# Optimization experiments

Measured on AMD Instinct MI355X. Metric: run time of the kernel, lower is better.

The kernel has to match this reference:

```python
import jax, jax.numpy as jnp
import numpy as np

KERNEL_EPS = 1e-3   # generalized_kernel epsilon (performer)
Z_EPS = 1e-6        # LinearHopfieldCore eps


def _phi(x, proj):
    # generalized_kernel with relu: phi(x) = relu(d^{-0.25} * x @ P^T) + 1e-3
    # x: [B, L, H, D], proj: [M, D] -> [B, L, H, M]
    scale = x.shape[-1] ** -0.25
    return jax.nn.relu(jnp.einsum('blhd,md->blhm', x * scale, proj)) + KERNEL_EPS


def setup_inputs() -> dict:
    key = jax.random.key(0)
    kq, kk, kv, kp = jax.random.split(key, 4)
    B, L, H, D, M = 4, 4096, 16, 64, 256
    return {
        'q': jax.random.normal(kq, (B, L, H, D), dtype=jnp.float32),
        'k': jax.random.normal(kk, (B, L, H, D), dtype=jnp.float32),
        'v': jax.random.normal(kv, (B, L, H, D), dtype=jnp.float32),
        'projection_matrix': jax.random.normal(kp, (M, D), dtype=jnp.float32),
    }


def reference(q, k, v, projection_matrix):
    # Feature maps [B, L, H, M]
    Qf = _phi(q, projection_matrix)
    Kf = _phi(k, projection_matrix)
    # Linear attention (non-causal):
    # KV = sum_s K_s otimes V_s : [B, H, M, E]
    KV = jnp.einsum('bshm,bshe->bhme', Kf, v)
    # Z = 1 / (Q . (sum_s K_s + eps)) : [B, H, L]
    Ksum = jnp.sum(Kf, axis=1) + Z_EPS        # [B, H, M]
    Z = 1.0 / jnp.einsum('blhm,bhm->bhl', Qf, Ksum)
    # out = (Q @ KV) * Z : [B, L, H, E]
    out = jnp.einsum('bhme,blhm,bhl->blhe', KV, Qf, Z)
    return out
```

## Files before the change

### kernel.cpp

```cpp
#include <hip/hip_runtime.h>


#define LL 4096
#define HH 16
#define DD 64
#define EE 64
#define MM 256
#define SCALE 0.35355339059327378f

typedef __attribute__((ext_vector_type(8))) __bf16 bf8v;
typedef __attribute__((ext_vector_type(4))) __bf16 bf4v;
typedef __attribute__((ext_vector_type(4))) float f4v;

__device__ __forceinline__ __bf16 f2bf(float f) {
  union { float f; unsigned u; } x; x.f = f;
  unsigned r = (x.u + 0x7FFFu + ((x.u >> 16) & 1u)) >> 16;
  union { unsigned short s; __bf16 b; } y; y.s = (unsigned short)r;
  return y.b;
}

#define MFMA16(a, b, c) __builtin_amdgcn_mfma_f32_16x16x32_bf16(a, b, c, 0, 0, 0)

#define KV_ELEMS (64 * 64 * 256)
#define KSUM_OFF KV_ELEMS
#define WS_ZERO_BYTES ((size_t)(KV_ELEMS + 64 * 256) * 4)

__global__ __launch_bounds__(256, 2)
void k1_kv(const float* __restrict__ kin, const float* __restrict__ vin,
           const float* __restrict__ pin, float* __restrict__ ws) {
  __shared__ __bf16 kt[64 * 72];
  __shared__ __bf16 vt[64 * 68];
  __shared__ __bf16 kft[256 * 72];

  const int tid = threadIdx.x;
  const int wave = tid >> 6;
  const int lane = tid & 63;
  const int qd = lane >> 4;
  const int nn = lane & 15;
  const int bh = blockIdx.y;
  const int b = bh >> 4, h = bh & 15;
  const int l0 = blockIdx.x * 512;

  bf8v pf[4][2];
#pragma unroll
  for (int mt = 0; mt < 4; ++mt) {
    const float* pr = pin + (size_t)(64 * wave + mt * 16 + nn) * DD;
#pragma unroll
    for (int c = 0; c < 2; ++c) {
      bf8v t;
#pragma unroll
      for (int j = 0; j < 8; ++j) t[j] = f2bf(pr[c * 32 + qd * 8 + j] * SCALE);
      pf[mt][c] = t;
    }
  }

  f4v acc[4][4];
#pragma unroll
  for (int i = 0; i < 4; ++i)
#pragma unroll
    for (int j = 0; j < 4; ++j) acc[i][j] = (f4v){0.f, 0.f, 0.f, 0.f};
  float ksum[4] = {0.f, 0.f, 0.f, 0.f};

  const size_t bhbase = (size_t)b * LL * HH * DD + (size_t)h * DD;
  const int srow = tid >> 2;
  const int scol = (tid & 3) * 16;

  for (int it = 0; it < 8; ++it) {
    {
      const size_t g = bhbase + (size_t)(l0 + it * 64 + srow) * (HH * DD) + scol;
      const f4v* gk = (const f4v*)(kin + g);
      const f4v* gv = (const f4v*)(vin + g);
      f4v k0 = gk[0], k1 = gk[1], k2 = gk[2], k3 = gk[3];
      f4v v0 = gv[0], v1 = gv[1], v2 = gv[2], v3 = gv[3];
      bf8v w0, w1;
#pragma unroll
      for (int j = 0; j < 4; ++j) {
        w0[j] = f2bf(k0[j]); w0[j + 4] = f2bf(k1[j]);
        w1[j] = f2bf(k2[j]); w1[j + 4] = f2bf(k3[j]);
      }
      *(bf8v*)&kt[srow * 72 + scol] = w0;
      *(bf8v*)&kt[srow * 72 + scol + 8] = w1;
      bf4v x0, x1, x2, x3;
#pragma unroll
      for (int j = 0; j < 4; ++j) {
        x0[j] = f2bf(v0[j]); x1[j] = f2bf(v1[j]);
        x2[j] = f2bf(v2[j]); x3[j] = f2bf(v3[j]);
      }
      *(bf4v*)&vt[srow * 68 + scol] = x0;
      *(bf4v*)&vt[srow * 68 + scol + 4] = x1;
      *(bf4v*)&vt[srow * 68 + scol + 8] = x2;
      *(bf4v*)&vt[srow * 68 + scol + 12] = x3;
    }
    __syncthreads();

#pragma unroll
    for (int lt = 0; lt < 4; ++lt) {
      bf8v a0 = *(const bf8v*)&kt[(lt * 16 + nn) * 72 + qd * 8];
      bf8v a1 = *(const bf8v*)&kt[(lt * 16 + nn) * 72 + 32 + qd * 8];
#pragma unroll
      for (int mt = 0; mt < 4; ++mt) {
        f4v cc = (f4v){0.f, 0.f, 0.f, 0.f};
        cc = MFMA16(a0, pf[mt][0], cc);
        cc = MFMA16(a1, pf[mt][1], cc);
        bf4v pk;
#pragma unroll
        for (int r = 0; r < 4; ++r) {
          float ph = fmaxf(cc[r], 0.f) + 1e-3f;
          ksum[mt] += ph;
          pk[r] = f2bf(ph);
        }
        *(bf4v*)&kft[(64 * wave + mt * 16 + nn) * 72 + lt * 16 + qd * 4] = pk;
      }
    }

#pragma unroll
    for (int c = 0; c < 2; ++c) {
      bf8v af[4];
#pragma unroll
      for (int mt = 0; mt < 4; ++mt)
        af[mt] = *(const bf8v*)&kft[(64 * wave + mt * 16 + nn) * 72 + c * 32 + qd * 8];
#pragma unroll
      for (int et = 0; et < 4; ++et) {
        bf8v bv;
#pragma unroll
        for (int j = 0; j < 8; ++j) bv[j] = vt[(c * 32 + qd * 8 + j) * 68 + et * 16 + nn];
#pragma unroll
        for (int mt = 0; mt < 4; ++mt) acc[mt][et] = MFMA16(af[mt], bv, acc[mt][et]);
      }
    }
    __syncthreads();
  }

  float* kvb = ws + (size_t)bh * (64 * 256);
#pragma unroll
  for (int mt = 0; mt < 4; ++mt)
#pragma unroll
    for (int et = 0; et < 4; ++et) {
#pragma unroll
      for (int r = 0; r < 4; ++r) {
        int m = 64 * wave + mt * 16 + 4 * qd + r;
        int e = et * 16 + nn;
        atomicAdd(&kvb[e * 256 + m], acc[mt][et][r]);
      }
    }
#pragma unroll
  for (int mt = 0; mt < 4; ++mt) {
    float s = ksum[mt];
    s += __shfl_xor(s, 16, 64);
    s += __shfl_xor(s, 32, 64);
    if (lane < 16) atomicAdd(&ws[KSUM_OFF + bh * 256 + 64 * wave + mt * 16 + lane], s);
  }
}

__global__ __launch_bounds__(256, 2)
void k3_out(const float* __restrict__ qin, const float* __restrict__ pin,
            const float* __restrict__ ws, float* __restrict__ out) {
  __shared__ __bf16 qt[64 * 72];
  __shared__ __bf16 qf[64 * 264];
  __shared__ float denp[256];
  __shared__ float denr[64];
  __shared__ float ksume[256];

  const int tid = threadIdx.x;
  const int wave = tid >> 6;
  const int lane = tid & 63;
  const int qd = lane >> 4;
  const int nn = lane & 15;
  const int bh = blockIdx.y;
  const int b = bh >> 4, h = bh & 15;
  const int l0 = blockIdx.x * 512;

  bf8v pf[4][2];
#pragma unroll
  for (int mt = 0; mt < 4; ++mt) {
    const float* pr = pin + (size_t)(64 * wave + mt * 16 + nn) * DD;
#pragma unroll
    for (int c = 0; c < 2; ++c) {
      bf8v t;
#pragma unroll
      for (int j = 0; j < 8; ++j) t[j] = f2bf(pr[c * 32 + qd * 8 + j] * SCALE);
      pf[mt][c] = t;
    }
  }

  const float* kvb = ws + (size_t)bh * (64 * 256);
  bf8v kvf[8];
#pragma unroll
  for (int c = 0; c < 8; ++c) {
    const float* src = kvb + (size_t)(16 * wave + nn) * 256 + c * 32 + qd * 8;
    bf8v t;
#pragma unroll
    for (int j = 0; j < 8; ++j) t[j] = f2bf(src[j]);
    kvf[c] = t;
  }

  ksume[tid] = ws[KSUM_OFF + bh * 256 + tid] + 1e-6f;

  const size_t bhbase = (size_t)b * LL * HH * DD + (size_t)h * DD;
  const int srow = tid >> 2;
  const int scol = (tid & 3) * 16;

  for (int it = 0; it < 8; ++it) {
    {
      const f4v* gq = (const f4v*)(qin + bhbase + (size_t)(l0 + it * 64 + srow) * (HH * DD) + scol);
      f4v q0 = gq[0], q1 = gq[1], q2 = gq[2], q3 = gq[3];
      bf8v w0, w1;
#pragma unroll
      for (int j = 0; j < 4; ++j) {
        w0[j] = f2bf(q0[j]); w0[j + 4] = f2bf(q1[j]);
        w1[j] = f2bf(q2[j]); w1[j + 4] = f2bf(q3[j]);
      }
      *(bf8v*)&qt[srow * 72 + scol] = w0;
      *(bf8v*)&qt[srow * 72 + scol + 8] = w1;
    }
    __syncthreads();

#pragma unroll
    for (int lt = 0; lt < 4; ++lt) {
      bf8v b0 = *(const bf8v*)&qt[(lt * 16 + nn) * 72 + qd * 8];
      bf8v b1 = *(const bf8v*)&qt[(lt * 16 + nn) * 72 + 32 + qd * 8];
      float dpart = 0.f;
#pragma unroll
      for (int mt = 0; mt < 4; ++mt) {
        f4v cc = (f4v){0.f, 0.f, 0.f, 0.f};
        cc = MFMA16(pf[mt][0], b0, cc);
        cc = MFMA16(pf[mt][1], b1, cc);
        bf4v pk;
#pragma unroll
        for (int r = 0; r < 4; ++r) {
          float ph = fmaxf(cc[r], 0.f) + 1e-3f;
          dpart += ph * ksume[64 * wave + mt * 16 + 4 * qd + r];
          pk[r] = f2bf(ph);
        }
        *(bf4v*)&qf[(lt * 16 + nn) * 264 + 64 * wave + mt * 16 + 4 * qd] = pk;
      }
      dpart += __shfl_xor(dpart, 16, 64);
      dpart += __shfl_xor(dpart, 32, 64);
      if (lane < 16) denp[wave * 64 + lt * 16 + lane] = dpart;
    }
    __syncthreads();
    if (tid < 64)
      denr[tid] = 1.f / (denp[tid] + denp[64 + tid] + denp[128 + tid] + denp[192 + tid]);
    __syncthreads();

#pragma unroll
    for (int lt = 0; lt < 4; ++lt) {
      f4v co = (f4v){0.f, 0.f, 0.f, 0.f};
#pragma unroll
      for (int c = 0; c < 8; ++c) {
        bf8v af = *(const bf8v*)&qf[(lt * 16 + nn) * 264 + c * 32 + qd * 8];
        co = MFMA16(af, kvf[c], co);
      }
#pragma unroll
      for (int r = 0; r < 4; ++r) {
        int lrel = lt * 16 + 4 * qd + r;
        int labs = l0 + it * 64 + lrel;
        out[((size_t)((size_t)b * LL + labs) * HH + h) * EE + 16 * wave + nn] =
            co[r] * denr[lrel];
      }
    }
    __syncthreads();
  }
}

extern "C" void kernel_launch(void* const* d_in, const int* in_sizes, int n_in,
                              void* d_out, int out_size, void* d_ws, size_t ws_size,
                              hipStream_t stream) {
  (void)in_sizes; (void)n_in; (void)out_size;
  const float* q = (const float*)d_in[0];
  const float* k = (const float*)d_in[1];
  const float* v = (const float*)d_in[2];
  const float* p = (const float*)d_in[3];
  float* ws = (float*)d_ws;
  float* out = (float*)d_out;

  if (ws_size < WS_ZERO_BYTES) return;

  hipMemsetAsync(d_ws, 0, WS_ZERO_BYTES, stream);
  dim3 grid(8, 64), blk(256);
  k1_kv<<<grid, blk, 0, stream>>>(k, v, p, ws);
  k3_out<<<grid, blk, 0, stream>>>(q, p, ws, out);
}
```

Before: 332.9 us.

## Double waves per block, prefetch next tile into registers, trim k3 barriers

Both kernels move from 4 to 8 waves per 512-thread block. In k1 each wave now owns 32 feature rows instead of 64. In k3 the waves split the L tiles, and each also covers its quarter of the E outputs. The global loads for the next 64-row tile are issued right after the barrier, so they overlap the MFMA work of the current tile. k3 also drops the separate reciprocal-denominator stage and the end-of-loop barrier, and each lane sums the four partial denominators itself. The aim is more latency hiding and fewer barrier stalls, at the cost of higher per-CU register pressure under the new launch bounds.

```diff
diff --git a/kernel.cpp b/kernel.cpp
--- a/kernel.cpp
+++ b/kernel.cpp
@@ -10,6 +10,7 @@
 
 typedef __attribute__((ext_vector_type(8))) __bf16 bf8v;
 typedef __attribute__((ext_vector_type(4))) __bf16 bf4v;
+typedef __attribute__((ext_vector_type(2))) __bf16 bf2v;
 typedef __attribute__((ext_vector_type(4))) float f4v;
 
 __device__ __forceinline__ __bf16 f2bf(float f) {
@@ -25,15 +26,15 @@
 #define KSUM_OFF KV_ELEMS
 #define WS_ZERO_BYTES ((size_t)(KV_ELEMS + 64 * 256) * 4)
 
-__global__ __launch_bounds__(256, 2)
+__global__ __launch_bounds__(512, 4)
 void k1_kv(const float* __restrict__ kin, const float* __restrict__ vin,
            const float* __restrict__ pin, float* __restrict__ ws) {
   __shared__ __bf16 kt[64 * 72];
-  __shared__ __bf16 vt[64 * 68];
+  __shared__ __bf16 vt[64 * 66];
   __shared__ __bf16 kft[256 * 72];
 
   const int tid = threadIdx.x;
-  const int wave = tid >> 6;
+  const int w = tid >> 6;
   const int lane = tid & 63;
   const int qd = lane >> 4;
   const int nn = lane & 15;
@@ -41,10 +42,19 @@
   const int b = bh >> 4, h = bh & 15;
   const int l0 = blockIdx.x * 512;
 
-  bf8v pf[4][2];
-#pragma unroll
-  for (int mt = 0; mt < 4; ++mt) {
-    const float* pr = pin + (size_t)(64 * wave + mt * 16 + nn) * DD;
+  const size_t bhbase = (size_t)b * LL * HH * DD + (size_t)h * DD;
+  const int srow = tid >> 3;
+  const int scol = (tid & 7) * 8;
+
+  const float* gk = kin + bhbase + (size_t)(l0 + srow) * (HH * DD) + scol;
+  const float* gv = vin + bhbase + (size_t)(l0 + srow) * (HH * DD) + scol;
+  f4v pk0 = ((const f4v*)gk)[0], pk1 = ((const f4v*)gk)[1];
+  f4v pv0 = ((const f4v*)gv)[0], pv1 = ((const f4v*)gv)[1];
+
+  bf8v pf[2][2];
+#pragma unroll
+  for (int mt = 0; mt < 2; ++mt) {
+    const float* pr = pin + (size_t)(32 * w + mt * 16 + nn) * DD;
 #pragma unroll
     for (int c = 0; c < 2; ++c) {
       bf8v t;
@@ -54,51 +64,42 @@
     }
   }
 
-  f4v acc[4][4];
-#pragma unroll
-  for (int i = 0; i < 4; ++i)
+  f4v acc[2][4];
+#pragma unroll
+  for (int i = 0; i < 2; ++i)
 #pragma unroll
     for (int j = 0; j < 4; ++j) acc[i][j] = (f4v){0.f, 0.f, 0.f, 0.f};
-  float ksum[4] = {0.f, 0.f, 0.f, 0.f};
-
-  const size_t bhbase = (size_t)b * LL * HH * DD + (size_t)h * DD;
-  const int srow = tid >> 2;
-  const int scol = (tid & 3) * 16;
+  float ksum[2] = {0.f, 0.f};
 
   for (int it = 0; it < 8; ++it) {
     {
-      const size_t g = bhbase + (size_t)(l0 + it * 64 + srow) * (HH * DD) + scol;
-      const f4v* gk = (const f4v*)(kin + g);
-      const f4v* gv = (const f4v*)(vin + g);
-      f4v k0 = gk[0], k1 = gk[1], k2 = gk[2], k3 = gk[3];
-      f4v v0 = gv[0], v1 = gv[1], v2 = gv[2], v3 = gv[3];
-      bf8v w0, w1;
-#pragma unroll
-      for (int j = 0; j < 4; ++j) {
-        w0[j] = f2bf(k0[j]); w0[j + 4] = f2bf(k1[j]);
-        w1[j] = f2bf(k2[j]); w1[j + 4] = f2bf(k3[j]);
-      }
-      *(bf8v*)&kt[srow * 72 + scol] = w0;
-      *(bf8v*)&kt[srow * 72 + scol + 8] = w1;
-      bf4v x0, x1, x2, x3;
-#pragma unroll
-      for (int j = 0; j < 4; ++j) {
-        x0[j] = f2bf(v0[j]); x1[j] = f2bf(v1[j]);
-        x2[j] = f2bf(v2[j]); x3[j] = f2bf(v3[j]);
-      }
-      *(bf4v*)&vt[srow * 68 + scol] = x0;
-      *(bf4v*)&vt[srow * 68 + scol + 4] = x1;
-      *(bf4v*)&vt[srow * 68 + scol + 8] = x2;
-      *(bf4v*)&vt[srow * 68 + scol + 12] = x3;
-    }
-    __syncthreads();
+      bf8v wk;
+#pragma unroll
+      for (int j = 0; j < 4; ++j) { wk[j] = f2bf(pk0[j]); wk[j + 4] = f2bf(pk1[j]); }
+      *(bf8v*)&kt[srow * 72 + scol] = wk;
+      bf2v x0 = {f2bf(pv0[0]), f2bf(pv0[1])};
+      bf2v x1 = {f2bf(pv0[2]), f2bf(pv0[3])};
+      bf2v x2 = {f2bf(pv1[0]), f2bf(pv1[1])};
+      bf2v x3 = {f2bf(pv1[2]), f2bf(pv1[3])};
+      *(bf2v*)&vt[srow * 66 + scol]     = x0;
+      *(bf2v*)&vt[srow * 66 + scol + 2] = x1;
+      *(bf2v*)&vt[srow * 66 + scol + 4] = x2;
+      *(bf2v*)&vt[srow * 66 + scol + 6] = x3;
+    }
+    __syncthreads();
+
+    if (it < 7) {
+      gk += 64 * HH * DD; gv += 64 * HH * DD;
+      pk0 = ((const f4v*)gk)[0]; pk1 = ((const f4v*)gk)[1];
+      pv0 = ((const f4v*)gv)[0]; pv1 = ((const f4v*)gv)[1];
+    }
 
 #pragma unroll
     for (int lt = 0; lt < 4; ++lt) {
       bf8v a0 = *(const bf8v*)&kt[(lt * 16 + nn) * 72 + qd * 8];
       bf8v a1 = *(const bf8v*)&kt[(lt * 16 + nn) * 72 + 32 + qd * 8];
 #pragma unroll
-      for (int mt = 0; mt < 4; ++mt) {
+      for (int mt = 0; mt < 2; ++mt) {
         f4v cc = (f4v){0.f, 0.f, 0.f, 0.f};
         cc = MFMA16(a0, pf[mt][0], cc);
         cc = MFMA16(a1, pf[mt][1], cc);
@@ -109,23 +110,21 @@
           ksum[mt] += ph;
           pk[r] = f2bf(ph);
         }
-        *(bf4v*)&kft[(64 * wave + mt * 16 + nn) * 72 + lt * 16 + qd * 4] = pk;
+        *(bf4v*)&kft[(32 * w + mt * 16 + nn) * 72 + lt * 16 + qd * 4] = pk;
       }
     }
 
 #pragma unroll
     for (int c = 0; c < 2; ++c) {
-      bf8v af[4];
-#pragma unroll
-      for (int mt = 0; mt < 4; ++mt)
-        af[mt] = *(const bf8v*)&kft[(64 * wave + mt * 16 + nn) * 72 + c * 32 + qd * 8];
+      bf8v af0 = *(const bf8v*)&kft[(32 * w + nn) * 72 + c * 32 + qd * 8];
+      bf8v af1 = *(const bf8v*)&kft[(32 * w + 16 + nn) * 72 + c * 32 + qd * 8];
 #pragma unroll
       for (int et = 0; et < 4; ++et) {
         bf8v bv;
 #pragma unroll
-        for (int j = 0; j < 8; ++j) bv[j] = vt[(c * 32 + qd * 8 + j) * 68 + et * 16 + nn];
-#pragma unroll
-        for (int mt = 0; mt < 4; ++mt) acc[mt][et] = MFMA16(af[mt], bv, acc[mt][et]);
+        for (int j = 0; j < 8; ++j) bv[j] = vt[(c * 32 + qd * 8 + j) * 66 + et * 16 + nn];
+        acc[0][et] = MFMA16(af0, bv, acc[0][et]);
+        acc[1][et] = MFMA16(af1, bv, acc[1][et]);
       }
     }
     __syncthreads();
@@ -133,47 +132,56 @@
 
   float* kvb = ws + (size_t)bh * (64 * 256);
 #pragma unroll
-  for (int mt = 0; mt < 4; ++mt)
+  for (int mt = 0; mt < 2; ++mt)
 #pragma unroll
     for (int et = 0; et < 4; ++et) {
 #pragma unroll
       for (int r = 0; r < 4; ++r) {
-        int m = 64 * wave + mt * 16 + 4 * qd + r;
+        int m = 32 * w + mt * 16 + 4 * qd + r;
         int e = et * 16 + nn;
         atomicAdd(&kvb[e * 256 + m], acc[mt][et][r]);
       }
     }
 #pragma unroll
-  for (int mt = 0; mt < 4; ++mt) {
+  for (int mt = 0; mt < 2; ++mt) {
     float s = ksum[mt];
     s += __shfl_xor(s, 16, 64);
     s += __shfl_xor(s, 32, 64);
-    if (lane < 16) atomicAdd(&ws[KSUM_OFF + bh * 256 + 64 * wave + mt * 16 + lane], s);
-  }
-}
-
-__global__ __launch_bounds__(256, 2)
+    if (lane < 16) atomicAdd(&ws[KSUM_OFF + bh * 256 + 32 * w + mt * 16 + lane], s);
+  }
+}
+
+__global__ __launch_bounds__(512, 4)
 void k3_out(const float* __restrict__ qin, const float* __restrict__ pin,
             const float* __restrict__ ws, float* __restrict__ out) {
   __shared__ __bf16 qt[64 * 72];
   __shared__ __bf16 qf[64 * 264];
   __shared__ float denp[256];
-  __shared__ float denr[64];
   __shared__ float ksume[256];
 
   const int tid = threadIdx.x;
-  const int wave = tid >> 6;
+  const int w = tid >> 6;
+  const int wm = w & 3;
+  const int wl = w >> 2;
   const int lane = tid & 63;
   const int qd = lane >> 4;
   const int nn = lane & 15;
   const int bh = blockIdx.y;
   const int b = bh >> 4, h = bh & 15;
   const int l0 = blockIdx.x * 512;
+  const int lt0 = 2 * wl;
+
+  const size_t bhbase = (size_t)b * LL * HH * DD + (size_t)h * DD;
+  const int srow = tid >> 3;
+  const int scol = (tid & 7) * 8;
+
+  const float* gq = qin + bhbase + (size_t)(l0 + srow) * (HH * DD) + scol;
+  f4v pq0 = ((const f4v*)gq)[0], pq1 = ((const f4v*)gq)[1];
 
   bf8v pf[4][2];
 #pragma unroll
   for (int mt = 0; mt < 4; ++mt) {
-    const float* pr = pin + (size_t)(64 * wave + mt * 16 + nn) * DD;
+    const float* pr = pin + (size_t)(64 * wm + mt * 16 + nn) * DD;
 #pragma unroll
     for (int c = 0; c < 2; ++c) {
       bf8v t;
@@ -187,36 +195,32 @@
   bf8v kvf[8];
 #pragma unroll
   for (int c = 0; c < 8; ++c) {
-    const float* src = kvb + (size_t)(16 * wave + nn) * 256 + c * 32 + qd * 8;
+    const float* src = kvb + (size_t)(16 * wm + nn) * 256 + c * 32 + qd * 8;
     bf8v t;
 #pragma unroll
     for (int j = 0; j < 8; ++j) t[j] = f2bf(src[j]);
     kvf[c] = t;
   }
 
-  ksume[tid] = ws[KSUM_OFF + bh * 256 + tid] + 1e-6f;
-
-  const size_t bhbase = (size_t)b * LL * HH * DD + (size_t)h * DD;
-  const int srow = tid >> 2;
-  const int scol = (tid & 3) * 16;
+  if (tid < 256) ksume[tid] = ws[KSUM_OFF + bh * 256 + tid] + 1e-6f;
 
   for (int it = 0; it < 8; ++it) {
     {
-      const f4v* gq = (const f4v*)(qin + bhbase + (size_t)(l0 + it * 64 + srow) * (HH * DD) + scol);
-      f4v q0 = gq[0], q1 = gq[1], q2 = gq[2], q3 = gq[3];
-      bf8v w0, w1;
-#pragma unroll
-      for (int j = 0; j < 4; ++j) {
-        w0[j] = f2bf(q0[j]); w0[j + 4] = f2bf(q1[j]);
-        w1[j] = f2bf(q2[j]); w1[j + 4] = f2bf(q3[j]);
-      }
-      *(bf8v*)&qt[srow * 72 + scol] = w0;
-      *(bf8v*)&qt[srow * 72 + scol + 8] = w1;
-    }
-    __syncthreads();
-
-#pragma unroll
-    for (int lt = 0; lt < 4; ++lt) {
+      bf8v wq;
+#pragma unroll
+      for (int j = 0; j < 4; ++j) { wq[j] = f2bf(pq0[j]); wq[j + 4] = f2bf(pq1[j]); }
+      *(bf8v*)&qt[srow * 72 + scol] = wq;
+    }
+    __syncthreads();
+
+    if (it < 7) {
+      gq += 64 * HH * DD;
+      pq0 = ((const f4v*)gq)[0]; pq1 = ((const f4v*)gq)[1];
+    }
+
+#pragma unroll
+    for (int li = 0; li < 2; ++li) {
+      const int lt = lt0 + li;
       bf8v b0 = *(const bf8v*)&qt[(lt * 16 + nn) * 72 + qd * 8];
       bf8v b1 = *(const bf8v*)&qt[(lt * 16 + nn) * 72 + 32 + qd * 8];
       float dpart = 0.f;
@@ -229,37 +233,39 @@
 #pragma unroll
         for (int r = 0; r < 4; ++r) {
           float ph = fmaxf(cc[r], 0.f) + 1e-3f;
-          dpart += ph * ksume[64 * wave + mt * 16 + 4 * qd + r];
+          dpart += ph * ksume[64 * wm + mt * 16 + 4 * qd + r];
           pk[r] = f2bf(ph);
         }
-        *(bf4v*)&qf[(lt * 16 + nn) * 264 + 64 * wave + mt * 16 + 4 * qd] = pk;
+        *(bf4v*)&qf[(lt * 16 + nn) * 264 + 64 * wm + mt * 16 + 4 * qd] = pk;
       }
       dpart += __shfl_xor(dpart, 16, 64);
       dpart += __shfl_xor(dpart, 32, 64);
-      if (lane < 16) denp[wave * 64 + lt * 16 + lane] = dpart;
-    }
-    __syncthreads();
-    if (tid < 64)
-      denr[tid] = 1.f / (denp[tid] + denp[64 + tid] + denp[128 + tid] + denp[192 + tid]);
-    __syncthreads();
-
-#pragma unroll
-    for (int lt = 0; lt < 4; ++lt) {
+      if (lane < 16) denp[wm * 64 + lt * 16 + lane] = dpart;
+    }
+    __syncthreads();
+
+#pragma unroll
+    for (int li = 0; li < 2; ++li) {
+      const int lt = lt0 + li;
       f4v co = (f4v){0.f, 0.f, 0.f, 0.f};
 #pragma unroll
       for (int c = 0; c < 8; ++c) {
         bf8v af = *(const bf8v*)&qf[(lt * 16 + nn) * 264 + c * 32 + qd * 8];
         co = MFMA16(af, kvf[c], co);
       }
+      f4v d0 = *(const f4v*)&denp[0 * 64 + lt * 16 + 4 * qd];
+      f4v d1 = *(const f4v*)&denp[1 * 64 + lt * 16 + 4 * qd];
+      f4v d2 = *(const f4v*)&denp[2 * 64 + lt * 16 + 4 * qd];
+      f4v d3 = *(const f4v*)&denp[3 * 64 + lt * 16 + 4 * qd];
 #pragma unroll
       for (int r = 0; r < 4; ++r) {
         int lrel = lt * 16 + 4 * qd + r;
         int labs = l0 + it * 64 + lrel;
-        out[((size_t)((size_t)b * LL + labs) * HH + h) * EE + 16 * wave + nn] =
-            co[r] * denr[lrel];
-      }
-    }
-    __syncthreads();
+        float rden = 1.f / (d0[r] + d1[r] + d2[r] + d3[r]);
+        out[((size_t)((size_t)b * LL + labs) * HH + h) * EE + 16 * wm + nn] =
+            co[r] * rden;
+      }
+    }
   }
 }
 
@@ -277,7 +283,7 @@
   if (ws_size < WS_ZERO_BYTES) return;
 
   hipMemsetAsync(d_ws, 0, WS_ZERO_BYTES, stream);
-  dim3 grid(8, 64), blk(256);
+  dim3 grid(8, 64), blk(512);
   k1_kv<<<grid, blk, 0, stream>>>(k, v, p, ws);
   k3_out<<<grid, blk, 0, stream>>>(q, p, ws, out);
 }
```

New measurement: 351.6 us. 5.6% more time.
